# Kernel tuning notes

Hardware: AMD Instinct MI355X
Metric: run time of the kernel (lower is better)

## Reference

```python
import jax, jax.numpy as jnp
import numpy as np

N = 8192
F_IN = 64
F_OUT = 64
ALPHA = 0.2  # LeakyReLU negative slope
NEG_INF = -9e15


def setup_inputs() -> dict:
    key = jax.random.key(0)
    k1, k2, k3, k4 = jax.random.split(key, 4)
    h = jax.random.normal(k1, (N, F_IN), dtype=jnp.float32)
    adj = jax.random.randint(k2, (N, N), 0, 2, dtype=jnp.int32)
    W = jax.random.normal(k3, (F_OUT, F_IN), dtype=jnp.float32) * (1.0 / np.sqrt(F_IN))
    a = jax.random.normal(k4, (2 * F_OUT,), dtype=jnp.float32) * (1.0 / np.sqrt(2 * F_OUT))
    return {"h": h, "adj": adj, "W": W, "a": a}


def reference(h, adj, W, a):
    # Wh = h @ W.T  (nn.Linear with no bias)
    Wh = h @ W.T  # [N, F_out]
    # The original builds [N*N, 2F] pairs then applies `a`; this is exactly
    # e_ij = leakyrelu(a1 . Wh_i + a2 . Wh_j) -- decomposed form, same math.
    a1, a2 = a[:F_OUT], a[F_OUT:]
    src = Wh @ a1  # [N]
    dst = Wh @ a2  # [N]
    e = jax.nn.leaky_relu(src[:, None] + dst[None, :], negative_slope=ALPHA)  # [N, N]
    scores = jnp.where(adj > 0, e, NEG_INF)
    attention = jax.nn.softmax(scores, axis=1)
    # dropout is identity in eval mode (dropout=0.0)
    h_prime = attention @ Wh  # [N, F_out]
    return jax.nn.elu(h_prime)
```

## Files before the change

### kernel.cpp

```cpp
#include <hip/hip_runtime.h>
#include <hip/hip_bf16.h>

#define NN 8192
#define F 64
#define ALPHA 0.2f
#define L2E 1.44269504f
#define DBOUND 16.0f
#define G 8
#define COLS (NN / G)
#define NSTEPS (COLS / 32)
#define RPB 128

typedef __attribute__((ext_vector_type(8))) short short8;
typedef __attribute__((ext_vector_type(4))) float f32x4;
typedef __attribute__((ext_vector_type(4))) int i32x4;

__device__ __forceinline__ unsigned fb(float x) {
    return __builtin_bit_cast(unsigned, x);
}
__device__ __forceinline__ short f2bf(float x) {
    union { float f; unsigned u; } v; v.f = x;
    unsigned r = v.u + 0x7FFF + ((v.u >> 16) & 1);
    return (short)(r >> 16);
}

__global__ __launch_bounds__(256) void k_prep(const float* __restrict__ h,
        const float* __restrict__ W, const float* __restrict__ a,
        short* __restrict__ WhTt, float* __restrict__ src, float* __restrict__ dst2) {
    __shared__ float Wl[F][F + 1];
    __shared__ short shT[F][4];
    int tid = threadIdx.x;
    for (int m = 0; m < 4; ++m) {
        int idx = m * 1024 + tid * 4;
        float4 v = *(const float4*)&W[idx];
        int row = idx >> 6, col = idx & 63;
        Wl[row][col] = v.x; Wl[row][col + 1] = v.y;
        Wl[row][col + 2] = v.z; Wl[row][col + 3] = v.w;
    }
    __syncthreads();
    int w = tid >> 6, lane = tid & 63;
    int i = blockIdx.x * 4 + w;
    const float* hrow = &h[(size_t)i * F];
    float wh = 0.f;
    #pragma unroll
    for (int k = 0; k < F; k += 4) {
        float4 hv = *(const float4*)&hrow[k];
        wh += hv.x * Wl[lane][k] + hv.y * Wl[lane][k + 1]
            + hv.z * Wl[lane][k + 2] + hv.w * Wl[lane][k + 3];
    }
    shT[lane][w] = f2bf(wh);
    float s1 = wh * a[lane];
    float s2 = wh * a[F + lane];
    #pragma unroll
    for (int off = 32; off; off >>= 1) {
        s1 += __shfl_xor(s1, off);
        s2 += __shfl_xor(s2, off);
    }
    if (lane == 0) { src[i] = s1; dst2[i] = s2 * L2E; }
    __syncthreads();
    if (tid < F) {
        int f = tid;
        int b = blockIdx.x;
        int t = b >> 3;
        int off = (b * 4) & 31;
        size_t addr = (((size_t)(t * 4 + (f >> 4)) * 64
                       + (off >> 3) * 16 + (f & 15)) << 3) + (off & 7);
        short4 v = make_short4(shT[f][0], shT[f][1], shT[f][2], shT[f][3]);
        *(short4*)&WhTt[addr] = v;
    }
}

__global__ __launch_bounds__(256) void k_mask(const int* __restrict__ adj,
                                              unsigned long long* __restrict__ mg) {
    int w = threadIdx.x >> 6, l = threadIdx.x & 63;
    int gw = blockIdx.x * 4 + w;
    const int NW = 2048 * 4;
    const int NCH = (NN * NN) / 256;
    int sh = 4 * (l & 15);
    #pragma unroll 4
    for (int c = gw; c < NCH; c += NW) {
        size_t base = (size_t)c * 256;
        i32x4 a = __builtin_nontemporal_load((const i32x4*)(adj + base) + l);
        unsigned n = (a.x > 0 ? 1u : 0u) | (a.y > 0 ? 2u : 0u)
                   | (a.z > 0 ? 4u : 0u) | (a.w > 0 ? 8u : 0u);
        unsigned long long v = (unsigned long long)n << sh;
        v |= __shfl_xor(v, 1);
        v |= __shfl_xor(v, 2);
        v |= __shfl_xor(v, 4);
        v |= __shfl_xor(v, 8);
        if ((l & 15) == 0)
            mg[base / 64 + (l >> 4)] = v;
    }
}

__global__ __launch_bounds__(512, 4) void k_attn(const unsigned* __restrict__ maskg,
        const short8* __restrict__ WhTt, const float* __restrict__ src,
        const float* __restrict__ dst2,
        float* __restrict__ Opart, float* __restrict__ lpart) {
    __shared__ unsigned mlds[RPB][33];
    __shared__ float e1lds[COLS];
    __shared__ float e2lds[COLS];

    int rb = blockIdx.x / G;
    int g  = blockIdx.x % G;
    int jbase = g * COLS;
    int tid = threadIdx.x;

    for (int idx = tid; idx < RPB * (COLS / 32); idx += 512) {
        int rr = idx >> 5, cc = idx & 31;
        mlds[rr][cc] = maskg[(size_t)(rb * RPB + rr) * (NN / 32) + (jbase >> 5) + cc];
    }
    for (int idx = tid; idx < COLS; idx += 512) {
        float d = dst2[jbase + idx];
        e1lds[idx] = __builtin_amdgcn_exp2f(d);
        e2lds[idx] = __builtin_amdgcn_exp2f(d * ALPHA);
    }
    __syncthreads();

    int w = tid >> 6, lane = tid & 63;
    int r = lane & 15, q = lane >> 4;
    int qs = q * 8;
    int i = rb * RPB + w * 16 + r;

    float srcv = src[i];
    float sM = srcv + DBOUND;
    float Mi = fmaxf(sM, ALPHA * sM);
    float sL  = srcv * L2E;
    float MiL = Mi * L2E;
    float eC1 = __builtin_amdgcn_exp2f(sL - MiL);
    float eC2 = __builtin_amdgcn_exp2f(fmaf(sL, ALPHA, -MiL));

    f32x4 acc0{}, acc1{}, acc2{}, acc3{}, acc4{};
    short8 ones;
    #pragma unroll
    for (int k = 0; k < 8; ++k) ones[k] = (short)0x3F80;

    const unsigned* mrow = &mlds[w * 16 + r][0];

#define LDB(tt, B0, B1, B2, B3) { \
    const short8* bp = WhTt + (size_t)(g * 32 + (tt)) * 256; \
    B0 = bp[lane]; B1 = bp[64 + lane]; B2 = bp[128 + lane]; B3 = bp[192 + lane]; }

#define PEL(u, v, bit, eo) { \
    float e = fmaxf(eC1 * (u), eC2 * (v)); \
    eo = (bit) ? e : 0.0f; }

    short8 cb0, cb1, cb2, cb3, nb0, nb1, nb2, nb3;
    LDB(0, cb0, cb1, cb2, cb3)
    unsigned cm = mrow[0];
    float4 cp0 = *(const float4*)&e1lds[qs];
    float4 cp1 = *(const float4*)&e1lds[qs + 4];
    float4 cq0 = *(const float4*)&e2lds[qs];
    float4 cq1 = *(const float4*)&e2lds[qs + 4];

    #pragma unroll 4
    for (int t = 0; t < NSTEPS; ++t) {
        int tn = (t + 1 < NSTEPS) ? t + 1 : t;
        LDB(tn, nb0, nb1, nb2, nb3)

        unsigned nm = mrow[tn];
        float4 np0 = *(const float4*)&e1lds[tn * 32 + qs];
        float4 np1 = *(const float4*)&e1lds[tn * 32 + qs + 4];
        float4 nq0 = *(const float4*)&e2lds[tn * 32 + qs];
        float4 nq1 = *(const float4*)&e2lds[tn * 32 + qs + 4];

        unsigned m8 = (cm >> qs) & 0xffu;
        float e0, e1, e2, e3, e4, e5, e6, e7;
        PEL(cp0.x, cq0.x, (m8 & 1u),   e0) PEL(cp0.y, cq0.y, (m8 & 2u),   e1)
        PEL(cp0.z, cq0.z, (m8 & 4u),   e2) PEL(cp0.w, cq0.w, (m8 & 8u),   e3)
        PEL(cp1.x, cq1.x, (m8 & 16u),  e4) PEL(cp1.y, cq1.y, (m8 & 32u),  e5)
        PEL(cp1.z, cq1.z, (m8 & 64u),  e6) PEL(cp1.w, cq1.w, (m8 & 128u), e7)

        unsigned w0 = __builtin_amdgcn_perm(fb(e1), fb(e0), 0x07060302u);
        unsigned w1 = __builtin_amdgcn_perm(fb(e3), fb(e2), 0x07060302u);
        unsigned w2 = __builtin_amdgcn_perm(fb(e5), fb(e4), 0x07060302u);
        unsigned w3 = __builtin_amdgcn_perm(fb(e7), fb(e6), 0x07060302u);
        short8 af = __builtin_bit_cast(short8, make_uint4(w0, w1, w2, w3));

        acc0 = __builtin_amdgcn_mfma_f32_16x16x32_bf16(af, cb0, acc0, 0, 0, 0);
        acc1 = __builtin_amdgcn_mfma_f32_16x16x32_bf16(af, cb1, acc1, 0, 0, 0);
        acc2 = __builtin_amdgcn_mfma_f32_16x16x32_bf16(af, cb2, acc2, 0, 0, 0);
        acc3 = __builtin_amdgcn_mfma_f32_16x16x32_bf16(af, cb3, acc3, 0, 0, 0);
        acc4 = __builtin_amdgcn_mfma_f32_16x16x32_bf16(af, ones, acc4, 0, 0, 0);

        cb0 = nb0; cb1 = nb1; cb2 = nb2; cb3 = nb3;
        cm = nm;
        cp0 = np0; cp1 = np1; cq0 = nq0; cq1 = nq1;
    }
#undef PEL
#undef LDB

    int ic = rb * RPB + w * 16 + q * 4;
    if (r == 0) {
        #pragma unroll
        for (int reg = 0; reg < 4; ++reg)
            lpart[(size_t)g * NN + ic + reg] = acc4[reg];
    }

    size_t ob = (size_t)g * (size_t)(NN * F);
    #pragma unroll
    for (int reg = 0; reg < 4; ++reg) {
        size_t ro = ob + (size_t)(ic + reg) * F + r;
        Opart[ro]      = acc0[reg];
        Opart[ro + 16] = acc1[reg];
        Opart[ro + 32] = acc2[reg];
        Opart[ro + 48] = acc3[reg];
    }
}

__global__ __launch_bounds__(256) void k_reduce(const float* __restrict__ Opart,
        const float* __restrict__ lpart, float* __restrict__ out) {
    int idx = blockIdx.x * 256 + threadIdx.x;
    int i = idx >> 6;
    float o = 0.f, l = 0.f;
    #pragma unroll
    for (int g = 0; g < G; ++g) {
        o += Opart[(size_t)g * (NN * F) + idx];
        l += lpart[(size_t)g * NN + i];
    }
    float hp = o / l;
    out[idx] = hp > 0.f ? hp : __expf(hp) - 1.f;
}

extern "C" void kernel_launch(void* const* d_in, const int* in_sizes, int n_in,
                              void* d_out, int out_size, void* d_ws, size_t ws_size,
                              hipStream_t stream) {
    const float* h  = (const float*)d_in[0];
    const int* adj  = (const int*)d_in[1];
    const float* W  = (const float*)d_in[2];
    const float* a  = (const float*)d_in[3];
    float* out = (float*)d_out;

    char* ws = (char*)d_ws;
    const size_t OFF_WHTT = 0;
    const size_t OFF_SRC  = (1u << 20);
    const size_t OFF_DST  = OFF_SRC + (32u << 10);
    const size_t OFF_LP   = OFF_DST + (32u << 10);
    const size_t OFF_MASK = OFF_LP + (size_t)G * NN * 4;
    const size_t OFF_OP   = OFF_MASK + (size_t)NN * (NN / 8);

    short* WhTt  = (short*)(ws + OFF_WHTT);
    float* src   = (float*)(ws + OFF_SRC);
    float* dst2  = (float*)(ws + OFF_DST);
    float* lpart = (float*)(ws + OFF_LP);
    unsigned long long* maskg = (unsigned long long*)(ws + OFF_MASK);
    float* Opart = (float*)(ws + OFF_OP);

    k_mask<<<2048, 256, 0, stream>>>(adj, maskg);
    k_prep<<<NN / 4, 256, 0, stream>>>(h, W, a, WhTt, src, dst2);
    k_attn<<<(NN / RPB) * G, 512, 0, stream>>>((const unsigned*)maskg,
                                               (const short8*)WhTt, src, dst2,
                                               Opart, lpart);
    k_reduce<<<(NN * F) / 256, 256, 0, stream>>>(Opart, lpart, out);
}
```

Before: 89.06 us.

## Fuse adjacency bitmask packing into attention kernel with double-buffered streaming

Removes the separate mask-packing kernel and its bitmask buffer in workspace. The attention kernel now reads the int32 adjacency tile directly, packs it into bits in a double-buffered LDS ring, and overlaps loading the next column chunk with MFMA work on the current one. Block size and rows per block are halved to fit the new staging. This drops one launch and one round trip of the packed mask through global memory, at the cost of more per-iteration work and extra barriers inside the attention loop.

```diff
diff --git a/kernel.cpp b/kernel.cpp
--- a/kernel.cpp
+++ b/kernel.cpp
@@ -9,7 +9,7 @@
 #define G 8
 #define COLS (NN / G)
 #define NSTEPS (COLS / 32)
-#define RPB 128
+#define RPB 64
 
 typedef __attribute__((ext_vector_type(8))) short short8;
 typedef __attribute__((ext_vector_type(4))) float f32x4;
@@ -70,34 +70,11 @@
     }
 }
 
-__global__ __launch_bounds__(256) void k_mask(const int* __restrict__ adj,
-                                              unsigned long long* __restrict__ mg) {
-    int w = threadIdx.x >> 6, l = threadIdx.x & 63;
-    int gw = blockIdx.x * 4 + w;
-    const int NW = 2048 * 4;
-    const int NCH = (NN * NN) / 256;
-    int sh = 4 * (l & 15);
-    #pragma unroll 4
-    for (int c = gw; c < NCH; c += NW) {
-        size_t base = (size_t)c * 256;
-        i32x4 a = __builtin_nontemporal_load((const i32x4*)(adj + base) + l);
-        unsigned n = (a.x > 0 ? 1u : 0u) | (a.y > 0 ? 2u : 0u)
-                   | (a.z > 0 ? 4u : 0u) | (a.w > 0 ? 8u : 0u);
-        unsigned long long v = (unsigned long long)n << sh;
-        v |= __shfl_xor(v, 1);
-        v |= __shfl_xor(v, 2);
-        v |= __shfl_xor(v, 4);
-        v |= __shfl_xor(v, 8);
-        if ((l & 15) == 0)
-            mg[base / 64 + (l >> 4)] = v;
-    }
-}
-
-__global__ __launch_bounds__(512, 4) void k_attn(const unsigned* __restrict__ maskg,
+__global__ __launch_bounds__(256, 4) void k_attn(const int* __restrict__ adj,
         const short8* __restrict__ WhTt, const float* __restrict__ src,
         const float* __restrict__ dst2,
         float* __restrict__ Opart, float* __restrict__ lpart) {
-    __shared__ unsigned mlds[RPB][33];
+    __shared__ unsigned mbuf[2][RPB][9];
     __shared__ float e1lds[COLS];
     __shared__ float e2lds[COLS];
 
@@ -105,19 +82,37 @@
     int g  = blockIdx.x % G;
     int jbase = g * COLS;
     int tid = threadIdx.x;
-
-    for (int idx = tid; idx < RPB * (COLS / 32); idx += 512) {
-        int rr = idx >> 5, cc = idx & 31;
-        mlds[rr][cc] = maskg[(size_t)(rb * RPB + rr) * (NN / 32) + (jbase >> 5) + cc];
-    }
-    for (int idx = tid; idx < COLS; idx += 512) {
+    int w = tid >> 6, lane = tid & 63;
+
+    for (int idx = tid; idx < COLS; idx += 256) {
         float d = dst2[jbase + idx];
         e1lds[idx] = __builtin_amdgcn_exp2f(d);
         e2lds[idx] = __builtin_amdgcn_exp2f(d * ALPHA);
     }
-    __syncthreads();
-
-    int w = tid >> 6, lane = tid & 63;
+
+    const int* arow0 = adj + (size_t)(rb * RPB) * NN + jbase;
+    int sh8 = 4 * (lane & 7);
+
+#define AISSUE(rr, cc, dst) \
+    dst = __builtin_nontemporal_load( \
+        (const i32x4*)(arow0 + (size_t)(rr) * NN + (size_t)(cc) * 256) + lane);
+
+#define APACK(av, rr, buf) { \
+    unsigned n = (av.x > 0 ? 1u : 0u) | (av.y > 0 ? 2u : 0u) \
+               | (av.z > 0 ? 4u : 0u) | (av.w > 0 ? 8u : 0u); \
+    unsigned v = n << sh8; \
+    v |= __shfl_xor(v, 1); v |= __shfl_xor(v, 2); v |= __shfl_xor(v, 4); \
+    if ((lane & 7) == 0) mbuf[buf][rr][lane >> 3] = v; }
+
+    #pragma unroll
+    for (int k0 = 0; k0 < 16; k0 += 4) {
+        i32x4 a0, a1, a2, a3;
+        AISSUE(w * 16 + k0,     0, a0) AISSUE(w * 16 + k0 + 1, 0, a1)
+        AISSUE(w * 16 + k0 + 2, 0, a2) AISSUE(w * 16 + k0 + 3, 0, a3)
+        APACK(a0, w * 16 + k0,     0) APACK(a1, w * 16 + k0 + 1, 0)
+        APACK(a2, w * 16 + k0 + 2, 0) APACK(a3, w * 16 + k0 + 3, 0)
+    }
+
     int r = lane & 15, q = lane >> 4;
     int qs = q * 8;
     int i = rb * RPB + w * 16 + r;
@@ -135,8 +130,6 @@
     #pragma unroll
     for (int k = 0; k < 8; ++k) ones[k] = (short)0x3F80;
 
-    const unsigned* mrow = &mlds[w * 16 + r][0];
-
 #define LDB(tt, B0, B1, B2, B3) { \
     const short8* bp = WhTt + (size_t)(g * 32 + (tt)) * 256; \
     B0 = bp[lane]; B1 = bp[64 + lane]; B2 = bp[128 + lane]; B3 = bp[192 + lane]; }
@@ -147,48 +140,66 @@
 
     short8 cb0, cb1, cb2, cb3, nb0, nb1, nb2, nb3;
     LDB(0, cb0, cb1, cb2, cb3)
-    unsigned cm = mrow[0];
-    float4 cp0 = *(const float4*)&e1lds[qs];
-    float4 cp1 = *(const float4*)&e1lds[qs + 4];
-    float4 cq0 = *(const float4*)&e2lds[qs];
-    float4 cq1 = *(const float4*)&e2lds[qs + 4];
-
-    #pragma unroll 4
-    for (int t = 0; t < NSTEPS; ++t) {
-        int tn = (t + 1 < NSTEPS) ? t + 1 : t;
-        LDB(tn, nb0, nb1, nb2, nb3)
-
-        unsigned nm = mrow[tn];
-        float4 np0 = *(const float4*)&e1lds[tn * 32 + qs];
-        float4 np1 = *(const float4*)&e1lds[tn * 32 + qs + 4];
-        float4 nq0 = *(const float4*)&e2lds[tn * 32 + qs];
-        float4 nq1 = *(const float4*)&e2lds[tn * 32 + qs + 4];
-
-        unsigned m8 = (cm >> qs) & 0xffu;
-        float e0, e1, e2, e3, e4, e5, e6, e7;
-        PEL(cp0.x, cq0.x, (m8 & 1u),   e0) PEL(cp0.y, cq0.y, (m8 & 2u),   e1)
-        PEL(cp0.z, cq0.z, (m8 & 4u),   e2) PEL(cp0.w, cq0.w, (m8 & 8u),   e3)
-        PEL(cp1.x, cq1.x, (m8 & 16u),  e4) PEL(cp1.y, cq1.y, (m8 & 32u),  e5)
-        PEL(cp1.z, cq1.z, (m8 & 64u),  e6) PEL(cp1.w, cq1.w, (m8 & 128u), e7)
-
-        unsigned w0 = __builtin_amdgcn_perm(fb(e1), fb(e0), 0x07060302u);
-        unsigned w1 = __builtin_amdgcn_perm(fb(e3), fb(e2), 0x07060302u);
-        unsigned w2 = __builtin_amdgcn_perm(fb(e5), fb(e4), 0x07060302u);
-        unsigned w3 = __builtin_amdgcn_perm(fb(e7), fb(e6), 0x07060302u);
-        short8 af = __builtin_bit_cast(short8, make_uint4(w0, w1, w2, w3));
-
-        acc0 = __builtin_amdgcn_mfma_f32_16x16x32_bf16(af, cb0, acc0, 0, 0, 0);
-        acc1 = __builtin_amdgcn_mfma_f32_16x16x32_bf16(af, cb1, acc1, 0, 0, 0);
-        acc2 = __builtin_amdgcn_mfma_f32_16x16x32_bf16(af, cb2, acc2, 0, 0, 0);
-        acc3 = __builtin_amdgcn_mfma_f32_16x16x32_bf16(af, cb3, acc3, 0, 0, 0);
-        acc4 = __builtin_amdgcn_mfma_f32_16x16x32_bf16(af, ones, acc4, 0, 0, 0);
-
-        cb0 = nb0; cb1 = nb1; cb2 = nb2; cb3 = nb3;
-        cm = nm;
-        cp0 = np0; cp1 = np1; cq0 = nq0; cq1 = nq1;
+    __syncthreads();
+
+    i32x4 sa0, sa1;
+    for (int c = 0; c < 4; ++c) {
+        int buf = c & 1, nbuf = buf ^ 1;
+        bool stg = (c < 3);
+        const unsigned* mrow = &mbuf[buf][w * 16 + r][0];
+
+        #pragma unroll
+        for (int ts = 0; ts < 8; ++ts) {
+            int t = c * 8 + ts;
+            if (stg && ts >= 1) {
+                APACK(sa0, (ts - 1) * 8 + w * 2,     nbuf)
+                APACK(sa1, (ts - 1) * 8 + w * 2 + 1, nbuf)
+            }
+            if (stg) {
+                AISSUE(ts * 8 + w * 2,     c + 1, sa0)
+                AISSUE(ts * 8 + w * 2 + 1, c + 1, sa1)
+            }
+
+            int tn = (t + 1 < NSTEPS) ? t + 1 : t;
+            LDB(tn, nb0, nb1, nb2, nb3)
+
+            unsigned m8 = (mrow[ts] >> qs) & 0xffu;
+            float4 p0 = *(const float4*)&e1lds[t * 32 + qs];
+            float4 p1 = *(const float4*)&e1lds[t * 32 + qs + 4];
+            float4 q0 = *(const float4*)&e2lds[t * 32 + qs];
+            float4 q1 = *(const float4*)&e2lds[t * 32 + qs + 4];
+
+            float e0, e1, e2, e3, e4, e5, e6, e7;
+            PEL(p0.x, q0.x, (m8 & 1u),   e0) PEL(p0.y, q0.y, (m8 & 2u),   e1)
+            PEL(p0.z, q0.z, (m8 & 4u),   e2) PEL(p0.w, q0.w, (m8 & 8u),   e3)
+            PEL(p1.x, q1.x, (m8 & 16u),  e4) PEL(p1.y, q1.y, (m8 & 32u),  e5)
+            PEL(p1.z, q1.z, (m8 & 64u),  e6) PEL(p1.w, q1.w, (m8 & 128u), e7)
+
+            unsigned w0 = __builtin_amdgcn_perm(fb(e1), fb(e0), 0x07060302u);
+            unsigned w1 = __builtin_amdgcn_perm(fb(e3), fb(e2), 0x07060302u);
+            unsigned w2 = __builtin_amdgcn_perm(fb(e5), fb(e4), 0x07060302u);
+            unsigned w3 = __builtin_amdgcn_perm(fb(e7), fb(e6), 0x07060302u);
+            short8 af = __builtin_bit_cast(short8, make_uint4(w0, w1, w2, w3));
+
+            acc0 = __builtin_amdgcn_mfma_f32_16x16x32_bf16(af, cb0, acc0, 0, 0, 0);
+            acc1 = __builtin_amdgcn_mfma_f32_16x16x32_bf16(af, cb1, acc1, 0, 0, 0);
+            acc2 = __builtin_amdgcn_mfma_f32_16x16x32_bf16(af, cb2, acc2, 0, 0, 0);
+            acc3 = __builtin_amdgcn_mfma_f32_16x16x32_bf16(af, cb3, acc3, 0, 0, 0);
+            acc4 = __builtin_amdgcn_mfma_f32_16x16x32_bf16(af, ones, acc4, 0, 0, 0);
+
+            cb0 = nb0; cb1 = nb1; cb2 = nb2; cb3 = nb3;
+
+            if (stg && ts == 7) {
+                APACK(sa0, 7 * 8 + w * 2,     nbuf)
+                APACK(sa1, 7 * 8 + w * 2 + 1, nbuf)
+            }
+        }
+        __syncthreads();
     }
 #undef PEL
 #undef LDB
+#undef APACK
+#undef AISSUE
 
     int ic = rb * RPB + w * 16 + q * 4;
     if (r == 0) {
@@ -236,20 +247,16 @@
     const size_t OFF_SRC  = (1u << 20);
     const size_t OFF_DST  = OFF_SRC + (32u << 10);
     const size_t OFF_LP   = OFF_DST + (32u << 10);
-    const size_t OFF_MASK = OFF_LP + (size_t)G * NN * 4;
-    const size_t OFF_OP   = OFF_MASK + (size_t)NN * (NN / 8);
+    const size_t OFF_OP   = OFF_LP + (size_t)G * NN * 4;
 
     short* WhTt  = (short*)(ws + OFF_WHTT);
     float* src   = (float*)(ws + OFF_SRC);
     float* dst2  = (float*)(ws + OFF_DST);
     float* lpart = (float*)(ws + OFF_LP);
-    unsigned long long* maskg = (unsigned long long*)(ws + OFF_MASK);
     float* Opart = (float*)(ws + OFF_OP);
 
-    k_mask<<<2048, 256, 0, stream>>>(adj, maskg);
     k_prep<<<NN / 4, 256, 0, stream>>>(h, W, a, WhTt, src, dst2);
-    k_attn<<<(NN / RPB) * G, 512, 0, stream>>>((const unsigned*)maskg,
-                                               (const short8*)WhTt, src, dst2,
+    k_attn<<<(NN / RPB) * G, 256, 0, stream>>>(adj, (const short8*)WhTt, src, dst2,
                                                Opart, lpart);
     k_reduce<<<(NN * F) / 256, 256, 0, stream>>>(Opart, lpart, out);
 }
```

Result: faster. 78.40 us (median of 2 runs) (-12.0%).
